# Kernel optimization log

Hardware: AMD Instinct MI355X
Metric: run time of the kernel (lower is better)

## Reference

```python
import jax, jax.numpy as jnp
import numpy as np

N_NODES = 50000
N_EDGES = 800000
D_IN = 64
D_RADIAL = 128


def setup_inputs() -> dict:
    key = jax.random.key(0)
    k1, k2, k3, k4, k5 = jax.random.split(key, 5)
    x = jax.random.normal(k1, (N_NODES, D_IN), dtype=jnp.float32)
    edge_basis = jax.random.normal(k2, (N_EDGES, D_RADIAL), dtype=jnp.float32)
    src = jax.random.randint(k3, (N_EDGES,), 0, N_NODES, dtype=jnp.int32)
    dst = jax.random.randint(k4, (N_EDGES,), 0, N_NODES, dtype=jnp.int32)
    # kaiming normal fan_in, linear nonlinearity: std = 1/sqrt(fan_in)
    W = jax.random.normal(k5, (D_IN, D_RADIAL), dtype=jnp.float32) / jnp.sqrt(
        jnp.float32(D_RADIAL))
    b = jnp.zeros((D_IN,), dtype=jnp.float32)
    return {"x": x, "edge_basis": edge_basis, "src": src, "dst": dst,
            "W": W, "b": b}


def reference(x, edge_basis, src, dst, W, b):
    # per-edge radial filter: Linear(d_radial -> d_in)  [E, d_in]
    filt = jnp.einsum('er,dr->ed', edge_basis, W) + b
    # gather source node features, multiply by filter  [E, d_in]
    m = x[src] * filt
    # scatter-sum messages into destination nodes      [N, d_in]
    h = jax.ops.segment_sum(m, dst, num_segments=x.shape[0])
    return h
```

## Files before the change

kernel.cpp:

```cpp
#include <hip/hip_runtime.h>

#define N_NODES  50000
#define N_EDGES  800000
#define D_IN     64
#define D_RADIAL 128
#define NTILES   (N_EDGES / 64)

typedef __bf16 bf16x8 __attribute__((ext_vector_type(8)));
typedef float  f32x4  __attribute__((ext_vector_type(4)));
typedef short  s16x8  __attribute__((ext_vector_type(8)));

__device__ inline unsigned int pack_bf16_pair(float lo, float hi) {
    return __builtin_amdgcn_perm(__float_as_uint(hi), __float_as_uint(lo), 0x07060302u);
}

__device__ inline unsigned short f2bf_rne(float f) {
    unsigned int u = __float_as_uint(f);
    u += 0x7FFFu + ((u >> 16) & 1u);
    return (unsigned short)(u >> 16);
}

__device__ inline int mini(int a, int b) { return a < b ? a : b; }

constexpr size_t ws_align(size_t x) { return (x + 255) & ~(size_t)255; }
constexpr size_t WS_CNT  = 0;
constexpr size_t WS_OFF  = ws_align(WS_CNT  + (size_t)N_NODES * 4);
constexpr size_t WS_CUR  = ws_align(WS_OFF  + (size_t)(N_NODES + 1) * 4);
constexpr size_t WS_BSUM = ws_align(WS_CUR  + (size_t)N_NODES * 4);
constexpr size_t WS_EORD = ws_align(WS_BSUM + 512);
constexpr size_t WS_SSRC = ws_align(WS_EORD + (size_t)N_EDGES * 4);
constexpr size_t WS_REQUIRED = WS_SSRC + (size_t)N_EDGES * 4;

#define SCAN_B    512
#define SCAN_NBLK ((N_NODES + SCAN_B - 1) / SCAN_B)
static_assert(SCAN_NBLK <= 128, "scan_tops assumes <=128 blocks");

__global__ __launch_bounds__(256) void hist_kernel(const int* __restrict__ dst,
                                                   int* __restrict__ cnt) {
    int i = blockIdx.x * 256 + threadIdx.x;
    if (i < N_EDGES) atomicAdd(&cnt[dst[i]], 1);
}

__global__ __launch_bounds__(SCAN_B) void scan_block(const int* __restrict__ cnt,
                                                     int* __restrict__ offs,
                                                     int* __restrict__ bsum) {
    const int t = threadIdx.x, b = blockIdx.x;
    const int i = b * SCAN_B + t;
    int v = (i < N_NODES) ? cnt[i] : 0;
    __shared__ int s[SCAN_B];
    s[t] = v;
    __syncthreads();
    for (int o = 1; o < SCAN_B; o <<= 1) {
        int add = (t >= o) ? s[t - o] : 0;
        __syncthreads();
        s[t] += add;
        __syncthreads();
    }
    if (i < N_NODES) offs[i] = s[t];
    if (t == SCAN_B - 1) bsum[b] = s[t];
}

__global__ __launch_bounds__(128) void scan_tops(int* __restrict__ bsum) {
    const int t = threadIdx.x;
    __shared__ int s[128];
    int v = (t < SCAN_NBLK) ? bsum[t] : 0;
    s[t] = v;
    __syncthreads();
    for (int o = 1; o < 128; o <<= 1) {
        int add = (t >= o) ? s[t - o] : 0;
        __syncthreads();
        s[t] += add;
        __syncthreads();
    }
    if (t < SCAN_NBLK) bsum[t] = s[t] - v;
}

__global__ __launch_bounds__(SCAN_B) void finalize_off(const int* __restrict__ cnt,
                                                       int* __restrict__ offs,
                                                       const int* __restrict__ bsum,
                                                       int* __restrict__ cur) {
    const int i = blockIdx.x * SCAN_B + threadIdx.x;
    if (i < N_NODES) {
        int e = offs[i] - cnt[i] + bsum[blockIdx.x];
        offs[i] = e;
        cur[i]  = e;
    }
    if (i == 0) offs[N_NODES] = N_EDGES;
}

__global__ __launch_bounds__(256) void scatter_build(const int* __restrict__ dst,
                                                     const int* __restrict__ src,
                                                     int* __restrict__ cur,
                                                     int* __restrict__ eord,
                                                     int* __restrict__ ssrc) {
    int i = blockIdx.x * 256 + threadIdx.x;
    if (i < N_EDGES) {
        int pos = atomicAdd(&cur[dst[i]], 1);
        eord[pos] = i;
        ssrc[pos] = src[i];
    }
}

__global__ __launch_bounds__(256) void node_kernel(
    const float* __restrict__ x,
    const float* __restrict__ eb,
    const int*   __restrict__ eord,
    const int*   __restrict__ ssrc,
    const int*   __restrict__ offs,
    const float* __restrict__ W,
    const float* __restrict__ bias_p,
    float*       __restrict__ out)
{
    const int lane = threadIdx.x & 63;
    const int wv   = threadIdx.x >> 6;
    const int l15  = lane & 15;
    const int quad = lane >> 4;

    bf16x8 wfrag[4][4];
    #pragma unroll
    for (int nt = 0; nt < 4; ++nt) {
        const int d = nt * 16 + l15;
        #pragma unroll
        for (int kt = 0; kt < 4; ++kt) {
            const float* p = W + d * D_RADIAL + kt * 32 + quad * 8;
            s16x8 s;
            #pragma unroll
            for (int j = 0; j < 8; ++j) s[j] = (short)f2bf_rne(p[j]);
            wfrag[nt][kt] = __builtin_bit_cast(bf16x8, s);
        }
    }
    float bv[4];
    #pragma unroll
    for (int nt = 0; nt < 4; ++nt) bv[nt] = bias_p[nt * 16 + l15];

    const int wid = blockIdx.x * 4 + wv;
    const int nw  = gridDim.x * 4;
    for (int n = wid; n < N_NODES; n += nw) {
        const int j0 = offs[n], j1 = offs[n + 1];

        float nacc[4] = {0.f, 0.f, 0.f, 0.f};

        for (int p0 = j0; p0 < j1; p0 += 16) {
            const int last = j1 - 1;

            const int e = eord[mini(p0 + l15, last)];
            int sr[4];
            #pragma unroll
            for (int reg = 0; reg < 4; ++reg)
                sr[reg] = ssrc[mini(p0 + quad * 4 + reg, last)];

            float xv[4][4];
            #pragma unroll
            for (int reg = 0; reg < 4; ++reg) {
                const float* xrow = x + (long)sr[reg] * D_IN;
                #pragma unroll
                for (int nt = 0; nt < 4; ++nt)
                    xv[reg][nt] = xrow[nt * 16 + l15];
            }

            f32x4 acc[4];
            #pragma unroll
            for (int nt = 0; nt < 4; ++nt) acc[nt] = (f32x4){0.f, 0.f, 0.f, 0.f};

            const float* pbase = eb + (long)e * D_RADIAL + quad * 8;
            #pragma unroll
            for (int kt = 0; kt < 4; ++kt) {
                f32x4 a0 = *(const f32x4*)(pbase + kt * 32);
                f32x4 a1 = *(const f32x4*)(pbase + kt * 32 + 4);
                int4 packed;
                packed.x = pack_bf16_pair(a0[0], a0[1]);
                packed.y = pack_bf16_pair(a0[2], a0[3]);
                packed.z = pack_bf16_pair(a1[0], a1[1]);
                packed.w = pack_bf16_pair(a1[2], a1[3]);
                bf16x8 afrag = __builtin_bit_cast(bf16x8, packed);
                #pragma unroll
                for (int nt = 0; nt < 4; ++nt)
                    acc[nt] = __builtin_amdgcn_mfma_f32_16x16x32_bf16(
                        afrag, wfrag[nt][kt], acc[nt], 0, 0, 0);
            }

            #pragma unroll
            for (int reg = 0; reg < 4; ++reg) {
                const bool rv = (p0 + quad * 4 + reg) < j1;
                #pragma unroll
                for (int nt = 0; nt < 4; ++nt) {
                    const float val = (acc[nt][reg] + bv[nt]) * xv[reg][nt];
                    nacc[nt] += rv ? val : 0.f;
                }
            }
        }

        #pragma unroll
        for (int nt = 0; nt < 4; ++nt) {
            nacc[nt] += __shfl_xor(nacc[nt], 16, 64);
            nacc[nt] += __shfl_xor(nacc[nt], 32, 64);
        }
        if (quad == 0) {
            float* orow = out + (size_t)n * D_IN;
            #pragma unroll
            for (int nt = 0; nt < 4; ++nt)
                orow[nt * 16 + l15] = nacc[nt];
        }
    }
}

__global__ __launch_bounds__(256) void edge_msg_kernel(
    const float* __restrict__ x,
    const float* __restrict__ eb,
    const int*   __restrict__ src,
    const int*   __restrict__ dst,
    const float* __restrict__ W,
    const float* __restrict__ bias_p,
    float*       __restrict__ out)
{
    const int lane = threadIdx.x & 63;
    const int wv   = threadIdx.x >> 6;
    const int l15  = lane & 15;
    const int quad = lane >> 4;

    bf16x8 wfrag[4][4];
    #pragma unroll
    for (int nt = 0; nt < 4; ++nt) {
        const int d = nt * 16 + l15;
        #pragma unroll
        for (int kt = 0; kt < 4; ++kt) {
            const float* p = W + d * D_RADIAL + kt * 32 + quad * 8;
            s16x8 s;
            #pragma unroll
            for (int j = 0; j < 8; ++j) s[j] = (short)f2bf_rne(p[j]);
            wfrag[nt][kt] = __builtin_bit_cast(bf16x8, s);
        }
    }
    float bv[4];
    #pragma unroll
    for (int nt = 0; nt < 4; ++nt) bv[nt] = bias_p[nt * 16 + l15];

    for (int tile = blockIdx.x; tile < NTILES; tile += gridDim.x) {
        const int ebase = tile * 64 + wv * 16;

        f32x4 acc[4];
        #pragma unroll
        for (int nt = 0; nt < 4; ++nt) acc[nt] = (f32x4){0.f, 0.f, 0.f, 0.f};

        #pragma unroll
        for (int kt = 0; kt < 4; ++kt) {
            const float* p = eb + (long)(ebase + l15) * D_RADIAL + kt * 32 + quad * 8;
            f32x4 a0 = *(const f32x4*)(p);
            f32x4 a1 = *(const f32x4*)(p + 4);
            int4 packed;
            packed.x = pack_bf16_pair(a0[0], a0[1]);
            packed.y = pack_bf16_pair(a0[2], a0[3]);
            packed.z = pack_bf16_pair(a1[0], a1[1]);
            packed.w = pack_bf16_pair(a1[2], a1[3]);
            bf16x8 afrag = __builtin_bit_cast(bf16x8, packed);
            #pragma unroll
            for (int nt = 0; nt < 4; ++nt)
                acc[nt] = __builtin_amdgcn_mfma_f32_16x16x32_bf16(
                    afrag, wfrag[nt][kt], acc[nt], 0, 0, 0);
        }

        const int erow = ebase + quad * 4;
        #pragma unroll
        for (int reg = 0; reg < 4; ++reg) {
            const int e  = erow + reg;
            const int sv = src[e];
            const int dv = dst[e];
            const float* xrow = x   + (long)sv * D_IN;
            float*       orow = out + (long)dv * D_IN;
            #pragma unroll
            for (int nt = 0; nt < 4; ++nt) {
                const int d = nt * 16 + l15;
                const float val = (acc[nt][reg] + bv[nt]) * xrow[d];
                unsafeAtomicAdd(orow + d, val);
            }
        }
    }
}

extern "C" void kernel_launch(void* const* d_in, const int* in_sizes, int n_in,
                              void* d_out, int out_size, void* d_ws, size_t ws_size,
                              hipStream_t stream) {
    const float* x    = (const float*)d_in[0];
    const float* eb   = (const float*)d_in[1];
    const int*   src  = (const int*)d_in[2];
    const int*   dst  = (const int*)d_in[3];
    const float* W    = (const float*)d_in[4];
    const float* bias = (const float*)d_in[5];
    float* out = (float*)d_out;

    if (ws_size >= WS_REQUIRED) {
        char* ws   = (char*)d_ws;
        int*  cnt  = (int*)(ws + WS_CNT);
        int*  offs = (int*)(ws + WS_OFF);
        int*  cur  = (int*)(ws + WS_CUR);
        int*  bsum = (int*)(ws + WS_BSUM);
        int*  eord = (int*)(ws + WS_EORD);
        int*  ssrc = (int*)(ws + WS_SSRC);

        hipMemsetAsync(cnt, 0, (size_t)N_NODES * 4, stream);
        hist_kernel   <<<(N_EDGES + 255) / 256, 256, 0, stream>>>(dst, cnt);
        scan_block    <<<SCAN_NBLK, SCAN_B, 0, stream>>>(cnt, offs, bsum);
        scan_tops     <<<1, 128, 0, stream>>>(bsum);
        finalize_off  <<<SCAN_NBLK, SCAN_B, 0, stream>>>(cnt, offs, bsum, cur);
        scatter_build <<<(N_EDGES + 255) / 256, 256, 0, stream>>>(dst, src, cur, eord, ssrc);
        node_kernel   <<<2560, 256, 0, stream>>>(x, eb, eord, ssrc, offs, W, bias, out);
    } else {
        hipMemsetAsync(d_out, 0, (size_t)N_NODES * D_IN * sizeof(float), stream);
        edge_msg_kernel<<<1024, 256, 0, stream>>>(x, eb, src, dst, W, bias, out);
    }
}
```

Measured before the change: 688.9 us.

## Replace per-node CSR walk with dst-sorted fixed edge tiles and segmented atomics

Instead of one wavefront per destination node looping over its CSR segment (average degree 16, with uneven tails and partially masked 16-edge tiles), each wavefront now processes a fixed 16-edge slice of the dst-sorted edge list. When all 16 edges share a destination it reduces them and does one atomic add per column. Otherwise it does segmented runs within each lane's 4 rows and issues atomics at run boundaries. This evens out the load and removes wasted MFMA work on padded tiles. In exchange it adds an output memset, an extra sorted-dst array write and read, and float atomics that make summation order nondeterministic.

```diff
diff --git a/kernel.cpp b/kernel.cpp
--- a/kernel.cpp
+++ b/kernel.cpp
@@ -19,8 +19,6 @@
     u += 0x7FFFu + ((u >> 16) & 1u);
     return (unsigned short)(u >> 16);
 }
-
-__device__ inline int mini(int a, int b) { return a < b ? a : b; }
 
 constexpr size_t ws_align(size_t x) { return (x + 255) & ~(size_t)255; }
 constexpr size_t WS_CNT  = 0;
@@ -29,7 +27,8 @@
 constexpr size_t WS_BSUM = ws_align(WS_CUR  + (size_t)N_NODES * 4);
 constexpr size_t WS_EORD = ws_align(WS_BSUM + 512);
 constexpr size_t WS_SSRC = ws_align(WS_EORD + (size_t)N_EDGES * 4);
-constexpr size_t WS_REQUIRED = WS_SSRC + (size_t)N_EDGES * 4;
+constexpr size_t WS_SDST = ws_align(WS_SSRC + (size_t)N_EDGES * 4);
+constexpr size_t WS_REQUIRED = WS_SDST + (size_t)N_EDGES * 4;
 
 #define SCAN_B    512
 #define SCAN_NBLK ((N_NODES + SCAN_B - 1) / SCAN_B)
@@ -92,21 +91,24 @@
                                                      const int* __restrict__ src,
                                                      int* __restrict__ cur,
                                                      int* __restrict__ eord,
-                                                     int* __restrict__ ssrc) {
+                                                     int* __restrict__ ssrc,
+                                                     int* __restrict__ sdst) {
     int i = blockIdx.x * 256 + threadIdx.x;
     if (i < N_EDGES) {
-        int pos = atomicAdd(&cur[dst[i]], 1);
+        int d   = dst[i];
+        int pos = atomicAdd(&cur[d], 1);
         eord[pos] = i;
         ssrc[pos] = src[i];
-    }
-}
-
-__global__ __launch_bounds__(256) void node_kernel(
+        sdst[pos] = d;
+    }
+}
+
+__global__ __launch_bounds__(256) void sorted_edge_kernel(
     const float* __restrict__ x,
     const float* __restrict__ eb,
     const int*   __restrict__ eord,
     const int*   __restrict__ ssrc,
-    const int*   __restrict__ offs,
+    const int*   __restrict__ sdst,
     const float* __restrict__ W,
     const float* __restrict__ bias_p,
     float*       __restrict__ out)
@@ -133,73 +135,76 @@
     #pragma unroll
     for (int nt = 0; nt < 4; ++nt) bv[nt] = bias_p[nt * 16 + l15];
 
-    const int wid = blockIdx.x * 4 + wv;
-    const int nw  = gridDim.x * 4;
-    for (int n = wid; n < N_NODES; n += nw) {
-        const int j0 = offs[n], j1 = offs[n + 1];
-
-        float nacc[4] = {0.f, 0.f, 0.f, 0.f};
-
-        for (int p0 = j0; p0 < j1; p0 += 16) {
-            const int last = j1 - 1;
-
-            const int e = eord[mini(p0 + l15, last)];
-            int sr[4];
-            #pragma unroll
-            for (int reg = 0; reg < 4; ++reg)
-                sr[reg] = ssrc[mini(p0 + quad * 4 + reg, last)];
-
-            float xv[4][4];
-            #pragma unroll
-            for (int reg = 0; reg < 4; ++reg) {
-                const float* xrow = x + (long)sr[reg] * D_IN;
+    for (int tile = blockIdx.x; tile < NTILES; tile += gridDim.x) {
+        const int ebase = tile * 64 + wv * 16;
+        const int erow  = ebase + quad * 4;
+
+        const int ea  = eord[ebase + l15];
+        const int4 s4 = *(const int4*)(ssrc + erow);
+        const int4 n4 = *(const int4*)(sdst + erow);
+        const int sr[4]  = {s4.x, s4.y, s4.z, s4.w};
+        const int ndv[4] = {n4.x, n4.y, n4.z, n4.w};
+
+        float xv[4][4];
+        #pragma unroll
+        for (int reg = 0; reg < 4; ++reg) {
+            const float* xrow = x + (long)sr[reg] * D_IN;
+            #pragma unroll
+            for (int nt = 0; nt < 4; ++nt)
+                xv[reg][nt] = xrow[nt * 16 + l15];
+        }
+
+        f32x4 acc[4];
+        #pragma unroll
+        for (int nt = 0; nt < 4; ++nt) acc[nt] = (f32x4){0.f, 0.f, 0.f, 0.f};
+
+        const float* pbase = eb + (long)ea * D_RADIAL + quad * 8;
+        #pragma unroll
+        for (int kt = 0; kt < 4; ++kt) {
+            f32x4 a0 = *(const f32x4*)(pbase + kt * 32);
+            f32x4 a1 = *(const f32x4*)(pbase + kt * 32 + 4);
+            int4 packed;
+            packed.x = pack_bf16_pair(a0[0], a0[1]);
+            packed.y = pack_bf16_pair(a0[2], a0[3]);
+            packed.z = pack_bf16_pair(a1[0], a1[1]);
+            packed.w = pack_bf16_pair(a1[2], a1[3]);
+            bf16x8 afrag = __builtin_bit_cast(bf16x8, packed);
+            #pragma unroll
+            for (int nt = 0; nt < 4; ++nt)
+                acc[nt] = __builtin_amdgcn_mfma_f32_16x16x32_bf16(
+                    afrag, wfrag[nt][kt], acc[nt], 0, 0, 0);
+        }
+
+        const int n_first = __shfl(ndv[0], 0, 64);
+        const int n_last  = __shfl(ndv[3], 48, 64);
+        if (n_first == n_last) {
+            #pragma unroll
+            for (int nt = 0; nt < 4; ++nt) {
+                float s = (acc[nt][0] + bv[nt]) * xv[0][nt]
+                        + (acc[nt][1] + bv[nt]) * xv[1][nt]
+                        + (acc[nt][2] + bv[nt]) * xv[2][nt]
+                        + (acc[nt][3] + bv[nt]) * xv[3][nt];
+                s += __shfl_xor(s, 16, 64);
+                s += __shfl_xor(s, 32, 64);
+                if (quad == 0)
+                    unsafeAtomicAdd(out + (long)n_first * D_IN + nt * 16 + l15, s);
+            }
+        } else {
+            #pragma unroll
+            for (int nt = 0; nt < 4; ++nt) {
+                float a = (acc[nt][0] + bv[nt]) * xv[0][nt];
                 #pragma unroll
-                for (int nt = 0; nt < 4; ++nt)
-                    xv[reg][nt] = xrow[nt * 16 + l15];
+                for (int reg = 1; reg < 4; ++reg) {
+                    const float v = (acc[nt][reg] + bv[nt]) * xv[reg][nt];
+                    if (ndv[reg] == ndv[reg - 1]) {
+                        a += v;
+                    } else {
+                        unsafeAtomicAdd(out + (long)ndv[reg - 1] * D_IN + nt * 16 + l15, a);
+                        a = v;
+                    }
+                }
+                unsafeAtomicAdd(out + (long)ndv[3] * D_IN + nt * 16 + l15, a);
             }
-
-            f32x4 acc[4];
-            #pragma unroll
-            for (int nt = 0; nt < 4; ++nt) acc[nt] = (f32x4){0.f, 0.f, 0.f, 0.f};
-
-            const float* pbase = eb + (long)e * D_RADIAL + quad * 8;
-            #pragma unroll
-            for (int kt = 0; kt < 4; ++kt) {
-                f32x4 a0 = *(const f32x4*)(pbase + kt * 32);
-                f32x4 a1 = *(const f32x4*)(pbase + kt * 32 + 4);
-                int4 packed;
-                packed.x = pack_bf16_pair(a0[0], a0[1]);
-                packed.y = pack_bf16_pair(a0[2], a0[3]);
-                packed.z = pack_bf16_pair(a1[0], a1[1]);
-                packed.w = pack_bf16_pair(a1[2], a1[3]);
-                bf16x8 afrag = __builtin_bit_cast(bf16x8, packed);
-                #pragma unroll
-                for (int nt = 0; nt < 4; ++nt)
-                    acc[nt] = __builtin_amdgcn_mfma_f32_16x16x32_bf16(
-                        afrag, wfrag[nt][kt], acc[nt], 0, 0, 0);
-            }
-
-            #pragma unroll
-            for (int reg = 0; reg < 4; ++reg) {
-                const bool rv = (p0 + quad * 4 + reg) < j1;
-                #pragma unroll
-                for (int nt = 0; nt < 4; ++nt) {
-                    const float val = (acc[nt][reg] + bv[nt]) * xv[reg][nt];
-                    nacc[nt] += rv ? val : 0.f;
-                }
-            }
-        }
-
-        #pragma unroll
-        for (int nt = 0; nt < 4; ++nt) {
-            nacc[nt] += __shfl_xor(nacc[nt], 16, 64);
-            nacc[nt] += __shfl_xor(nacc[nt], 32, 64);
-        }
-        if (quad == 0) {
-            float* orow = out + (size_t)n * D_IN;
-            #pragma unroll
-            for (int nt = 0; nt < 4; ++nt)
-                orow[nt * 16 + l15] = nacc[nt];
         }
     }
 }
@@ -296,14 +301,18 @@
         int*  bsum = (int*)(ws + WS_BSUM);
         int*  eord = (int*)(ws + WS_EORD);
         int*  ssrc = (int*)(ws + WS_SSRC);
+        int*  sdst = (int*)(ws + WS_SDST);
 
         hipMemsetAsync(cnt, 0, (size_t)N_NODES * 4, stream);
+        hipMemsetAsync(d_out, 0, (size_t)N_NODES * D_IN * sizeof(float), stream);
         hist_kernel   <<<(N_EDGES + 255) / 256, 256, 0, stream>>>(dst, cnt);
         scan_block    <<<SCAN_NBLK, SCAN_B, 0, stream>>>(cnt, offs, bsum);
         scan_tops     <<<1, 128, 0, stream>>>(bsum);
         finalize_off  <<<SCAN_NBLK, SCAN_B, 0, stream>>>(cnt, offs, bsum, cur);
-        scatter_build <<<(N_EDGES + 255) / 256, 256, 0, stream>>>(dst, src, cur, eord, ssrc);
-        node_kernel   <<<2560, 256, 0, stream>>>(x, eb, eord, ssrc, offs, W, bias, out);
+        scatter_build <<<(N_EDGES + 255) / 256, 256, 0, stream>>>(dst, src, cur,
+                                                                  eord, ssrc, sdst);
+        sorted_edge_kernel<<<1280, 256, 0, stream>>>(x, eb, eord, ssrc, sdst,
+                                                     W, bias, out);
     } else {
         hipMemsetAsync(d_out, 0, (size_t)N_NODES * D_IN * sizeof(float), stream);
         edge_msg_kernel<<<1024, 256, 0, stream>>>(x, eb, src, dst, W, bias, out);
```

Measured after the change: 717.9 us. +4.2%, slower.
